# Kernel optimization log

Hardware: AMD Instinct MI355X
Metric: run time of the kernel (lower is better)

## Reference

```python
import jax, jax.numpy as jnp
import numpy as np

NUM_NODES = 80000
V_GLOBALS = 50000
N = 32      # grapharea_size
D = 300     # feature dim
R = 4       # num relations
E = 64      # edges per timestep
B, T = 2, 64


def setup_inputs() -> dict:
    key = jax.random.key(0)
    ks = jax.random.split(key, 10)
    return {
        "x_indices": jax.random.randint(ks[0], (B, T, N), 0, NUM_NODES, dtype=jnp.int32),
        "edge_index": jax.random.randint(ks[1], (B, T, 2, E), 0, N, dtype=jnp.int32),
        "edge_type": jax.random.randint(ks[2], (B, T, E), 0, R, dtype=jnp.int32),
        "X": jax.random.normal(ks[3], (NUM_NODES, D), jnp.float32) * 0.1,
        "conv_W": jax.random.normal(ks[4], (R, D, D), jnp.float32) * (1.0 / np.sqrt(D)),
        "W_0": jax.random.normal(ks[5], (D, D), jnp.float32) * (1.0 / np.sqrt(D)),
        "update_gate_W": jax.random.normal(ks[6], (N * D, D), jnp.float32) * (1.0 / np.sqrt(N * D)),
        "update_gate_U": jax.random.normal(ks[7], (D, D), jnp.float32) * (1.0 / np.sqrt(D)),
        "lin_w": jax.random.normal(ks[8], (V_GLOBALS, D), jnp.float32) * (1.0 / np.sqrt(D)),
        "lin_b": jax.random.normal(ks[9], (V_GLOBALS,), jnp.float32) * 0.01,
    }


def _rgcn_step(X, conv_W, W_0, Wg, Ug, lin_w, lin_b, mem, idx, ei, et):
    # gather grapharea features: [N, D]
    gx = X[idx]
    src, dst = ei[0], ei[1]
    n = gx.shape[0]
    r = conv_W.shape[0]
    # per-relation linear transform: [R, N, D]
    xw = jnp.einsum('nd,rde->rne', gx, conv_W)
    # edge-type masks emulate split_edge_index: [R, E]
    mask = (et[None, :] == jnp.arange(r, dtype=et.dtype)[:, None]).astype(gx.dtype)
    # GCN symmetric normalization with self-loops (deg includes self-loop weight 1)
    deg = jax.vmap(lambda w: jax.ops.segment_sum(w, dst, num_segments=n))(mask) + 1.0  # [R, N]
    dis = jax.lax.rsqrt(deg)
    norm = dis[:, src] * dis[:, dst] * mask                      # [R, E]
    msgs = xw[:, src, :] * norm[..., None]                       # [R, E, D]
    agg = jax.vmap(lambda m: jax.ops.segment_sum(m, dst, num_segments=n))(msgs)
    agg = agg + xw * (dis ** 2)[..., None]                       # self-loop messages
    composite = agg.sum(0)                                       # sum over relations, [N, D]
    # eye(N) @ (gx @ W_0) == gx @ W_0
    proposed = composite + gx @ W_0
    # GRU-style update gate from flattened grapharea + previous memory's first node
    u = jax.nn.sigmoid(gx.reshape(-1) @ Wg + mem[0] @ Ug)        # [D]
    new = u[None, :] * proposed + (1.0 - u[None, :]) * mem       # [N, D]
    x1 = jax.nn.leaky_relu(new)[0]                               # current node, [D]
    logits = x1 @ lin_w.T + lin_b                                # [V]
    return new, jax.nn.log_softmax(logits)


def reference(x_indices, edge_index, edge_type, X, conv_W, W_0, update_gate_W, update_gate_U, lin_w, lin_b):
    b, t, n = x_indices.shape
    s = b * t
    idxs = x_indices.reshape(s, n)
    eis = edge_index.reshape(s, 2, -1)
    ets = edge_type.reshape(s, -1)

    def step(mem, inp):
        idx, ei, et = inp
        new, logp = _rgcn_step(X, conv_W, W_0, update_gate_W, update_gate_U,
                               lin_w, lin_b, mem, idx, ei, et)
        # memory carry is a non-grad buffer updated via .data.copy_ in torch
        return jax.lax.stop_gradient(new), logp

    mem0 = jnp.zeros((n, X.shape[1]), X.dtype)
    _, preds_globals = jax.lax.scan(step, mem0, (idxs, eis, ets))  # [S, V]
    preds_senses = jnp.zeros((s,), X.dtype)  # include_senses=False -> stacked zeros
    return preds_globals, preds_senses
```

## Files before the change

### kernel.cpp

```cpp
#include <hip/hip_runtime.h>

#define S 128
#define N 32
#define D 300
#define DP 320
#define E 64
#define R 4
#define V 50000
#define VP 50048
#define ND 9600
#define KY 1504
#define DPAD 304

typedef unsigned short ushortT;
typedef __attribute__((ext_vector_type(8))) short short8;
typedef __attribute__((ext_vector_type(4))) short short4v;
typedef __attribute__((ext_vector_type(4))) float floatx4;
typedef __attribute__((ext_vector_type(19))) float floatx19;

__device__ inline float bf2f(ushortT h) {
    unsigned u = ((unsigned)h) << 16;
    float f;
    __builtin_memcpy(&f, &u, 4);
    return f;
}

__device__ inline float bfbits_lo(unsigned u) {
    unsigned b = u << 16;
    float f;
    __builtin_memcpy(&f, &b, 4);
    return f;
}

__device__ inline float bfbits_hi(unsigned u) {
    unsigned b = u & 0xffff0000u;
    float f;
    __builtin_memcpy(&f, &b, 4);
    return f;
}

__device__ inline ushortT f2bf(float f) {
    unsigned u;
    __builtin_memcpy(&u, &f, 4);
    unsigned r = (u + 0x7fffu + ((u >> 16) & 1u)) >> 16;
    return (ushortT)r;
}

__device__ inline float ldf(const void* p, size_t i, int isb) {
    return isb ? bf2f(((const ushortT*)p)[i]) : ((const float*)p)[i];
}

__device__ inline float rdlane(float v, int lane) {
    int iv;
    __builtin_memcpy(&iv, &v, 4);
    int r = __builtin_amdgcn_readlane(iv, lane);
    float f;
    __builtin_memcpy(&f, &r, 4);
    return f;
}

__global__ void k_detect(const void* X, int* flag) {
    __shared__ int bad;
    if (threadIdx.x == 0) bad = 0;
    __syncthreads();
    const ushortT* p = (const ushortT*)X;
    int b = 0;
    for (int i = threadIdx.x; i < 4096; i += 256) {
        float v = bf2f(p[i]);
        if (!(v > -2.f && v < 2.f)) b = 1;
    }
    if (b) atomicOr(&bad, 1);
    __syncthreads();
    if (threadIdx.x == 0) flag[0] = bad ? 0 : 1;
}

__global__ void k_gatherb(const int* __restrict__ flag, const int* __restrict__ xi,
                          const void* __restrict__ X, ushortT* __restrict__ gxb) {
    int isb = flag[0];
    int sn = blockIdx.x;
    int d = threadIdx.x;
    if (d < D) {
        int node = xi[sn];
        ushortT v = isb ? ((const ushortT*)X)[(size_t)node * D + d]
                        : f2bf(((const float*)X)[(size_t)node * D + d]);
        gxb[(size_t)sn * D + d] = v;
    }
}

__global__ void k_twg(const int* __restrict__ flag, const void* __restrict__ Wg,
                      ushortT* __restrict__ wgt) {
    int isb = flag[0];
    __shared__ float tile[32][33];
    int k0 = blockIdx.x * 32, d0 = blockIdx.y * 32;
    int tx = threadIdx.x & 31, ty = threadIdx.x >> 5;
    for (int i = ty; i < 32; i += 8) {
        int d = d0 + tx;
        tile[i][tx] = (d < D) ? ldf(Wg, (size_t)(k0 + i) * D + d, isb) : 0.f;
    }
    __syncthreads();
    for (int i = ty; i < 32; i += 8) {
        int d = d0 + i;
        if (d < DPAD) wgt[(size_t)d * ND + k0 + tx] = f2bf(tile[tx][i]);
    }
}

__global__ void k_tws(const int* __restrict__ flag, const void* __restrict__ convW,
                      const void* __restrict__ W0, ushortT* __restrict__ wst) {
    int isb = flag[0];
    __shared__ float tile[32][33];
    int k0 = blockIdx.x * 32, d0 = blockIdx.y * 32;
    int tx = threadIdx.x & 31, ty = threadIdx.x >> 5;
    for (int i = ty; i < 32; i += 8) {
        int kp = k0 + i, d = d0 + tx;
        float v = 0.f;
        if (d < D && kp < 1500)
            v = (kp < 1200) ? ldf(convW, (size_t)kp * D + d, isb)
                            : ldf(W0, (size_t)(kp - 1200) * D + d, isb);
        tile[i][tx] = v;
    }
    __syncthreads();
    for (int i = ty; i < 32; i += 8) {
        int d = d0 + i;
        if (d < DPAD) wst[(size_t)d * KY + k0 + tx] = f2bf(tile[tx][i]);
    }
}

__global__ void k_yb(const ushortT* __restrict__ gxb, const int* __restrict__ ei,
                     const int* __restrict__ et, ushortT* __restrict__ yb) {
    int s = blockIdx.x;
    int t = threadIdx.x;
    __shared__ int se[E], de[E], te[E];
    __shared__ float disv[R][N];
    if (t < E) {
        se[t] = ei[(size_t)s * 2 * E + t];
        de[t] = ei[(size_t)s * 2 * E + E + t];
        te[t] = et[(size_t)s * E + t];
    }
    __syncthreads();
    if (t < R * N) {
        int r = t >> 5, n = t & 31;
        float c = 1.f;
        for (int e = 0; e < E; ++e) c += (te[e] == r && de[e] == n) ? 1.f : 0.f;
        disv[r][n] = rsqrtf(c);
    }
    __syncthreads();
    if (t < D) {
        const ushortT* g = gxb + (size_t)s * ND;
        float g0 = bf2f(g[t]);
        float yy[R];
#pragma unroll
        for (int r = 0; r < R; ++r) yy[r] = g0 * disv[r][0] * disv[r][0];
        for (int e = 0; e < E; ++e) {
            if (de[e] == 0) {
                int r = te[e];
                yy[r] += disv[r][se[e]] * disv[r][0] * bf2f(g[(size_t)se[e] * D + t]);
            }
        }
#pragma unroll
        for (int r = 0; r < R; ++r) yb[(size_t)s * KY + r * D + t] = f2bf(yy[r]);
        yb[(size_t)s * KY + 4 * D + t] = g[t];
    }
    if (t < 4) yb[(size_t)s * KY + 1500 + t] = 0;
}

__global__ __launch_bounds__(256) void k_gemm(const ushortT* __restrict__ A, int lda,
                                              const ushortT* __restrict__ Bt, int ldb,
                                              float* __restrict__ C, int ldc, int ncols,
                                              int kchunks, int per) {
    int wave = threadIdx.x >> 6, lane = threadIdx.x & 63;
    int col = lane & 15, quad = lane >> 4;
    int m0 = blockIdx.x * 16, n0 = blockIdx.y * 16;
    int z = blockIdx.z;
    int kbeg = z * per;
    int kend = kbeg + per;
    if (kend > kchunks) kend = kchunks;
    floatx4 acc = {0.f, 0.f, 0.f, 0.f};
    const ushortT* ap = A + (size_t)(m0 + col) * lda + quad * 8;
    const ushortT* bp = Bt + (size_t)(n0 + col) * ldb + quad * 8;
    for (int kc = kbeg + wave; kc < kend; kc += 4) {
        short8 a = *(const short8*)(ap + kc * 32);
        short8 b = *(const short8*)(bp + kc * 32);
        acc = __builtin_amdgcn_mfma_f32_16x16x32_bf16(a, b, acc, 0, 0, 0);
    }
    __shared__ float red[4][64][4];
#pragma unroll
    for (int i = 0; i < 4; ++i) red[wave][lane][i] = acc[i];
    __syncthreads();
    if (wave == 0) {
#pragma unroll
        for (int i = 0; i < 4; ++i) {
            float v = red[0][lane][i] + red[1][lane][i] + red[2][lane][i] + red[3][lane][i];
            int m = m0 + quad * 4 + i;
            int n = n0 + col;
            if (n < ncols) C[(size_t)z * S * ldc + (size_t)m * ldc + n] = v;
        }
    }
}

__global__ void k_red(const float* __restrict__ part, float* __restrict__ out, int n, int nz) {
    int i = blockIdx.x * 256 + threadIdx.x;
    if (i < n) {
        float v = 0.f;
        for (int z = 0; z < nz; ++z) v += part[(size_t)z * n + i];
        out[i] = v;
    }
}

__global__ __attribute__((amdgpu_flat_work_group_size(512, 512), amdgpu_waves_per_eu(2, 2))) void
k_scan(const int* __restrict__ flag, const float* __restrict__ a, const float* __restrict__ P0,
       const void* __restrict__ Ug, ushortT* __restrict__ x1p) {
    int isb = flag[0];
    int t = threadIdx.x;
    int w = t >> 6, lane = t & 63;
    int kbase = w * 38;
    int d4 = 256 + lane;
    bool d4ok = d4 < D;
    floatx19 A0, A1, A2, A3, A4, B0, B1, B2, B3, B4;
    if (isb) {
        const ushortT* U = (const ushortT*)Ug;
#pragma unroll
        for (int j = 0; j < 19; ++j) {
            int k1 = kbase + j, k2 = k1 + 19;
            bool k2ok = k2 < D;
            A0[j] = bf2f(U[k1 * D + lane]);
            A1[j] = bf2f(U[k1 * D + 64 + lane]);
            A2[j] = bf2f(U[k1 * D + 128 + lane]);
            A3[j] = bf2f(U[k1 * D + 192 + lane]);
            A4[j] = d4ok ? bf2f(U[k1 * D + d4]) : 0.f;
            B0[j] = k2ok ? bf2f(U[k2 * D + lane]) : 0.f;
            B1[j] = k2ok ? bf2f(U[k2 * D + 64 + lane]) : 0.f;
            B2[j] = k2ok ? bf2f(U[k2 * D + 128 + lane]) : 0.f;
            B3[j] = k2ok ? bf2f(U[k2 * D + 192 + lane]) : 0.f;
            B4[j] = (k2ok && d4ok) ? bf2f(U[k2 * D + d4]) : 0.f;
        }
    } else {
        const float* U = (const float*)Ug;
#pragma unroll
        for (int j = 0; j < 19; ++j) {
            int k1 = kbase + j, k2 = k1 + 19;
            bool k2ok = k2 < D;
            A0[j] = U[k1 * D + lane];
            A1[j] = U[k1 * D + 64 + lane];
            A2[j] = U[k1 * D + 128 + lane];
            A3[j] = U[k1 * D + 192 + lane];
            A4[j] = d4ok ? U[k1 * D + d4] : 0.f;
            B0[j] = k2ok ? U[k2 * D + lane] : 0.f;
            B1[j] = k2ok ? U[k2 * D + 64 + lane] : 0.f;
            B2[j] = k2ok ? U[k2 * D + 128 + lane] : 0.f;
            B3[j] = k2ok ? U[k2 * D + 192 + lane] : 0.f;
            B4[j] = (k2ok && d4ok) ? U[k2 * D + d4] : 0.f;
        }
    }
    __shared__ float msh[336];
    __shared__ float part[8][320];
    for (int i = t; i < 336; i += 512) msh[i] = 0.f;
    float mreg = 0.f;
    __syncthreads();
    for (int s = 0; s < S; ++s) {
        float av = 0.f, pv = 0.f;
        if (t < D) {
            av = a[s * D + t];
            pv = P0[s * D + t];
        }
        float chunk = msh[kbase + lane];
        float acc0 = 0.f, acc1 = 0.f, acc2 = 0.f, acc3 = 0.f, acc4 = 0.f;
#pragma unroll
        for (int j = 0; j < 19; ++j) {
            float sm = rdlane(chunk, j);
            acc0 = fmaf(sm, A0[j], acc0);
            acc1 = fmaf(sm, A1[j], acc1);
            acc2 = fmaf(sm, A2[j], acc2);
            acc3 = fmaf(sm, A3[j], acc3);
            acc4 = fmaf(sm, A4[j], acc4);
        }
#pragma unroll
        for (int j = 0; j < 19; ++j) {
            float sm = rdlane(chunk, 19 + j);
            acc0 = fmaf(sm, B0[j], acc0);
            acc1 = fmaf(sm, B1[j], acc1);
            acc2 = fmaf(sm, B2[j], acc2);
            acc3 = fmaf(sm, B3[j], acc3);
            acc4 = fmaf(sm, B4[j], acc4);
        }
        part[w][lane] = acc0;
        part[w][64 + lane] = acc1;
        part[w][128 + lane] = acc2;
        part[w][192 + lane] = acc3;
        part[w][256 + lane] = acc4;
        __syncthreads();
        if (t < 320) {
            float pr = 0.f;
#pragma unroll
            for (int w2 = 0; w2 < 8; ++w2) pr += part[w2][t];
            if (t < D) {
                float pre = av + pr;
                float u = 1.f / (1.f + __expf(-pre));
                float nm = u * pv + (1.f - u) * mreg;
                mreg = nm;
                msh[t] = nm;
                float x = nm > 0.f ? nm : 0.01f * nm;
                x1p[(size_t)s * DP + t] = f2bf(x);
            } else {
                x1p[(size_t)s * DP + t] = 0;
            }
        }
        __syncthreads();
    }
}

__global__ __launch_bounds__(256) void k_logits(const int* __restrict__ flag,
                                                const ushortT* __restrict__ x1p,
                                                const void* __restrict__ lw,
                                                const void* __restrict__ lb,
                                                void* __restrict__ out) {
    int isb = flag[0];
    int wave = threadIdx.x >> 6, lane = threadIdx.x & 63;
    int col = lane & 15, quad = lane >> 4;
    int v = blockIdx.x * 64 + wave * 16 + col;
    int vv = v < V ? v : V - 1;
    floatx4 acc[8];
#pragma unroll
    for (int i = 0; i < 8; ++i) acc[i] = (floatx4){0.f, 0.f, 0.f, 0.f};
#pragma unroll
    for (int kc = 0; kc < 9; ++kc) {
        int k0 = kc * 32 + quad * 8;
        short8 b;
        if (isb) {
            const ushortT* bp = (const ushortT*)lw + (size_t)vv * D + k0;
            short4v lo = *(const short4v*)bp;
            short4v hi = *(const short4v*)(bp + 4);
            b = (short8){lo[0], lo[1], lo[2], lo[3], hi[0], hi[1], hi[2], hi[3]};
        } else {
            const float* bp = (const float*)lw + (size_t)vv * D + k0;
            floatx4 f0 = *(const floatx4*)bp;
            floatx4 f1 = *(const floatx4*)(bp + 4);
            b = (short8){(short)f2bf(f0[0]), (short)f2bf(f0[1]), (short)f2bf(f0[2]),
                         (short)f2bf(f0[3]), (short)f2bf(f1[0]), (short)f2bf(f1[1]),
                         (short)f2bf(f1[2]), (short)f2bf(f1[3])};
        }
#pragma unroll
        for (int st = 0; st < 8; ++st) {
            short8 aa = *(const short8*)(x1p + (size_t)(st * 16 + col) * DP + k0);
            acc[st] = __builtin_amdgcn_mfma_f32_16x16x32_bf16(aa, b, acc[st], 0, 0, 0);
        }
    }
    {
        int k0 = 288 + quad * 8;
        short8 b;
#pragma unroll
        for (int j = 0; j < 8; ++j) {
            int k = k0 + j;
            ushortT bv = 0;
            if (k < D)
                bv = isb ? ((const ushortT*)lw)[(size_t)vv * D + k]
                         : f2bf(((const float*)lw)[(size_t)vv * D + k]);
            b[j] = (short)bv;
        }
#pragma unroll
        for (int st = 0; st < 8; ++st) {
            short8 aa = *(const short8*)(x1p + (size_t)(st * 16 + col) * DP + k0);
            acc[st] = __builtin_amdgcn_mfma_f32_16x16x32_bf16(aa, b, acc[st], 0, 0, 0);
        }
    }
    if (v < V) {
        float bias = ldf(lb, v, isb);
#pragma unroll
        for (int st = 0; st < 8; ++st) {
#pragma unroll
            for (int i = 0; i < 4; ++i) {
                int s = st * 16 + quad * 4 + i;
                float val = acc[st][i] + bias;
                if (isb)
                    ((ushortT*)out)[(size_t)s * V + v] = f2bf(val);
                else
                    ((float*)out)[(size_t)s * V + v] = val;
            }
        }
    }
}

__global__ __launch_bounds__(512) void k_norm(const int* __restrict__ flag,
                                              void* __restrict__ out) {
    int isb = flag[0];
    int s = blockIdx.x;
    int t = threadIdx.x;
    __shared__ float red[512];
    if (s == 0 && t < S) {
        if (isb)
            ((ushortT*)out)[(size_t)S * V + t] = 0;
        else
            ((float*)out)[(size_t)S * V + t] = 0.f;
    }
    float mx = -1e30f;
    if (isb) {
        const uint4* row = (const uint4*)((const ushortT*)out + (size_t)s * V);
        for (int i = t; i < 6250; i += 512) {
            uint4 q = row[i];
            mx = fmaxf(mx, fmaxf(fmaxf(bfbits_lo(q.x), bfbits_hi(q.x)),
                                 fmaxf(bfbits_lo(q.y), bfbits_hi(q.y))));
            mx = fmaxf(mx, fmaxf(fmaxf(bfbits_lo(q.z), bfbits_hi(q.z)),
                                 fmaxf(bfbits_lo(q.w), bfbits_hi(q.w))));
        }
    } else {
        const floatx4* row = (const floatx4*)((const float*)out + (size_t)s * V);
        for (int i = t; i < 12500; i += 512) {
            floatx4 q = row[i];
            mx = fmaxf(mx, fmaxf(fmaxf(q[0], q[1]), fmaxf(q[2], q[3])));
        }
    }
    red[t] = mx;
    __syncthreads();
    for (int o = 256; o > 0; o >>= 1) {
        if (t < o) red[t] = fmaxf(red[t], red[t + o]);
        __syncthreads();
    }
    float M = red[0];
    __syncthreads();
    float sm = 0.f;
    if (isb) {
        const uint4* row = (const uint4*)((const ushortT*)out + (size_t)s * V);
        for (int i = t; i < 6250; i += 512) {
            uint4 q = row[i];
            sm += __expf(bfbits_lo(q.x) - M) + __expf(bfbits_hi(q.x) - M) +
                  __expf(bfbits_lo(q.y) - M) + __expf(bfbits_hi(q.y) - M) +
                  __expf(bfbits_lo(q.z) - M) + __expf(bfbits_hi(q.z) - M) +
                  __expf(bfbits_lo(q.w) - M) + __expf(bfbits_hi(q.w) - M);
        }
    } else {
        const floatx4* row = (const floatx4*)((const float*)out + (size_t)s * V);
        for (int i = t; i < 12500; i += 512) {
            floatx4 q = row[i];
            sm += __expf(q[0] - M) + __expf(q[1] - M) + __expf(q[2] - M) + __expf(q[3] - M);
        }
    }
    red[t] = sm;
    __syncthreads();
    for (int o = 256; o > 0; o >>= 1) {
        if (t < o) red[t] += red[t + o];
        __syncthreads();
    }
    float lse = M + __logf(red[0]);
    if (isb) {
        uint4* row = (uint4*)((ushortT*)out + (size_t)s * V);
        for (int i = t; i < 6250; i += 512) {
            uint4 q = row[i];
            uint4 o;
            o.x = (unsigned)f2bf(bfbits_lo(q.x) - lse) |
                  ((unsigned)f2bf(bfbits_hi(q.x) - lse) << 16);
            o.y = (unsigned)f2bf(bfbits_lo(q.y) - lse) |
                  ((unsigned)f2bf(bfbits_hi(q.y) - lse) << 16);
            o.z = (unsigned)f2bf(bfbits_lo(q.z) - lse) |
                  ((unsigned)f2bf(bfbits_hi(q.z) - lse) << 16);
            o.w = (unsigned)f2bf(bfbits_lo(q.w) - lse) |
                  ((unsigned)f2bf(bfbits_hi(q.w) - lse) << 16);
            row[i] = o;
        }
    } else {
        floatx4* row = (floatx4*)((float*)out + (size_t)s * V);
        for (int i = t; i < 12500; i += 512) {
            floatx4 q = row[i];
            q[0] -= lse;
            q[1] -= lse;
            q[2] -= lse;
            q[3] -= lse;
            row[i] = q;
        }
    }
}

#define OFF_FLAG 0
#define OFF_GXB 256
#define OFF_WGT 2457856
#define OFF_WST 8294656
#define OFF_YB 9209088
#define OFF_A 9594112
#define OFF_P0 9747712
#define OFF_X1P 9901312
#define OFF_STATS 9983232
#define OFF_PART 9983744
#define PART_A_BYTES (4 * S * D * 4)
#define PART_P_BYTES (2 * S * D * 4)

extern "C" void kernel_launch(void* const* d_in, const int* in_sizes, int n_in, void* d_out,
                              int out_size, void* d_ws, size_t ws_size, hipStream_t stream) {
    const int* xi = (const int*)d_in[0];
    const int* ei = (const int*)d_in[1];
    const int* et = (const int*)d_in[2];
    const void* X = d_in[3];
    const void* convW = d_in[4];
    const void* W0 = d_in[5];
    const void* Wg = d_in[6];
    const void* Ug = d_in[7];
    const void* lw = d_in[8];
    const void* lb = d_in[9];
    char* ws = (char*)d_ws;

    int* flag = (int*)(ws + OFF_FLAG);
    ushortT* gxb = (ushortT*)(ws + OFF_GXB);
    ushortT* wgt = (ushortT*)(ws + OFF_WGT);
    ushortT* wst = (ushortT*)(ws + OFF_WST);
    ushortT* yb = (ushortT*)(ws + OFF_YB);
    float* a = (float*)(ws + OFF_A);
    float* P0 = (float*)(ws + OFF_P0);
    ushortT* x1p = (ushortT*)(ws + OFF_X1P);

    bool split = ws_size >= (size_t)(OFF_PART + PART_A_BYTES + PART_P_BYTES);
    int nza = split ? 4 : 1;
    int nzp = split ? 2 : 1;
    float* apart = split ? (float*)(ws + OFF_PART) : a;
    float* ppart = split ? (float*)(ws + OFF_PART + PART_A_BYTES) : P0;
    int pera = (ND / 32 + nza - 1) / nza;
    int perp = (KY / 32 + nzp - 1) / nzp;

    hipLaunchKernelGGL(k_detect, dim3(1), dim3(256), 0, stream, X, flag);
    hipLaunchKernelGGL(k_gatherb, dim3(S * N), dim3(DP), 0, stream, flag, xi, X, gxb);
    hipLaunchKernelGGL(k_twg, dim3(ND / 32, 10), dim3(256), 0, stream, flag, Wg, wgt);
    hipLaunchKernelGGL(k_tws, dim3(KY / 32, 10), dim3(256), 0, stream, flag, convW, W0, wst);
    hipLaunchKernelGGL(k_yb, dim3(S), dim3(DP), 0, stream, gxb, ei, et, yb);
    hipLaunchKernelGGL(k_gemm, dim3(S / 16, 19, nza), dim3(256), 0, stream, gxb, ND, wgt, ND,
                       apart, D, D, ND / 32, pera);
    if (split)
        hipLaunchKernelGGL(k_red, dim3((S * D + 255) / 256), dim3(256), 0, stream, apart, a,
                           S * D, nza);
    hipLaunchKernelGGL(k_gemm, dim3(S / 16, 19, nzp), dim3(256), 0, stream, yb, KY, wst, KY,
                       ppart, D, D, KY / 32, perp);
    if (split)
        hipLaunchKernelGGL(k_red, dim3((S * D + 255) / 256), dim3(256), 0, stream, ppart, P0,
                           S * D, nzp);
    hipLaunchKernelGGL(k_scan, dim3(1), dim3(512), 0, stream, flag, a, P0, Ug, x1p);
    hipLaunchKernelGGL(k_logits, dim3(VP / 64), dim3(256), 0, stream, flag, x1p, lw, lb, d_out);
    hipLaunchKernelGGL(k_norm, dim3(S), dim3(512), 0, stream, flag, d_out);
}
```

Measured before the change: 461.2 us.

## Remove second barrier in scan via double-buffered partials and lane-local state

```diff
diff --git a/kernel.cpp b/kernel.cpp
--- a/kernel.cpp
+++ b/kernel.cpp
@@ -213,6 +213,8 @@
     int t = threadIdx.x;
     int w = t >> 6, lane = t & 63;
     int kbase = w * 38;
+    int myk = kbase + lane;
+    bool red_ok = (lane < 38) && (myk < D);
     int d4 = 256 + lane;
     bool d4ok = d4 < D;
     floatx19 A0, A1, A2, A3, A4, B0, B1, B2, B3, B4;
@@ -251,22 +253,23 @@
             B4[j] = (k2ok && d4ok) ? U[k2 * D + d4] : 0.f;
         }
     }
-    __shared__ float msh[336];
-    __shared__ float part[8][320];
-    for (int i = t; i < 336; i += 512) msh[i] = 0.f;
+    for (int i = t; i < S * 20; i += 512) {
+        int s = i / 20, d = 300 + (i % 20);
+        x1p[(size_t)s * DP + d] = 0;
+    }
+    __shared__ float part[2][8][320];
     float mreg = 0.f;
-    __syncthreads();
+    int buf = 0;
     for (int s = 0; s < S; ++s) {
         float av = 0.f, pv = 0.f;
-        if (t < D) {
-            av = a[s * D + t];
-            pv = P0[s * D + t];
-        }
-        float chunk = msh[kbase + lane];
+        if (red_ok) {
+            av = a[s * D + myk];
+            pv = P0[s * D + myk];
+        }
         float acc0 = 0.f, acc1 = 0.f, acc2 = 0.f, acc3 = 0.f, acc4 = 0.f;
 #pragma unroll
         for (int j = 0; j < 19; ++j) {
-            float sm = rdlane(chunk, j);
+            float sm = rdlane(mreg, j);
             acc0 = fmaf(sm, A0[j], acc0);
             acc1 = fmaf(sm, A1[j], acc1);
             acc2 = fmaf(sm, A2[j], acc2);
@@ -275,36 +278,30 @@
         }
 #pragma unroll
         for (int j = 0; j < 19; ++j) {
-            float sm = rdlane(chunk, 19 + j);
+            float sm = rdlane(mreg, 19 + j);
             acc0 = fmaf(sm, B0[j], acc0);
             acc1 = fmaf(sm, B1[j], acc1);
             acc2 = fmaf(sm, B2[j], acc2);
             acc3 = fmaf(sm, B3[j], acc3);
             acc4 = fmaf(sm, B4[j], acc4);
         }
-        part[w][lane] = acc0;
-        part[w][64 + lane] = acc1;
-        part[w][128 + lane] = acc2;
-        part[w][192 + lane] = acc3;
-        part[w][256 + lane] = acc4;
+        part[buf][w][lane] = acc0;
+        part[buf][w][64 + lane] = acc1;
+        part[buf][w][128 + lane] = acc2;
+        part[buf][w][192 + lane] = acc3;
+        part[buf][w][256 + lane] = acc4;
         __syncthreads();
-        if (t < 320) {
-            float pr = 0.f;
-#pragma unroll
-            for (int w2 = 0; w2 < 8; ++w2) pr += part[w2][t];
-            if (t < D) {
-                float pre = av + pr;
-                float u = 1.f / (1.f + __expf(-pre));
-                float nm = u * pv + (1.f - u) * mreg;
-                mreg = nm;
-                msh[t] = nm;
-                float x = nm > 0.f ? nm : 0.01f * nm;
-                x1p[(size_t)s * DP + t] = f2bf(x);
-            } else {
-                x1p[(size_t)s * DP + t] = 0;
-            }
-        }
-        __syncthreads();
+        if (red_ok) {
+            float pr = av;
+#pragma unroll
+            for (int w2 = 0; w2 < 8; ++w2) pr += part[buf][w2][myk];
+            float u = 1.f / (1.f + __expf(-pr));
+            float nm = u * pv + (1.f - u) * mreg;
+            mreg = nm;
+            float x = nm > 0.f ? nm : 0.01f * nm;
+            x1p[(size_t)s * DP + myk] = f2bf(x);
+        }
+        buf ^= 1;
     }
 }
 
```

After: 463.0 us. About the same (+0.4%).
